# Kernel tuning notes

Measured on AMD Instinct MI355X. Metric: run time of the kernel, lower is better.

## Reference

```python
import jax, jax.numpy as jnp
import numpy as np
import math

D_MODEL = 1024
NUM_HEADS = 16
D_HEAD = D_MODEL // NUM_HEADS


def setup_inputs() -> dict:
    key = jax.random.key(0)
    k1, k2, k3, k4, k5 = jax.random.split(key, 5)
    scale = 1.0 / math.sqrt(D_MODEL)
    x = jax.random.normal(k1, (4, 2048, D_MODEL), dtype=jnp.float32)
    W_qkv = jax.random.normal(k2, (D_MODEL, 3 * D_MODEL), dtype=jnp.float32) * scale
    b_qkv = jax.random.normal(k3, (3 * D_MODEL,), dtype=jnp.float32) * 0.02
    W_o = jax.random.normal(k4, (D_MODEL, D_MODEL), dtype=jnp.float32) * scale
    b_o = jax.random.normal(k5, (D_MODEL,), dtype=jnp.float32) * 0.02
    return {"x": x, "W_qkv": W_qkv, "b_qkv": b_qkv, "W_o": W_o, "b_o": b_o}


def reference(x, W_qkv, b_qkv, W_o, b_o):
    B, C, D = x.shape
    H, Dh = NUM_HEADS, D_HEAD
    qkv = x @ W_qkv + b_qkv                       # [B, C, 3D]
    qkv = qkv.reshape(B, C, 3, H, Dh).transpose(2, 0, 3, 1, 4)  # [3, B, H, C, Dh]
    Q, K, V = qkv[0], qkv[1], qkv[2]
    scores = jnp.einsum('bhqd,bhkd->bhqk', Q, K) / math.sqrt(Dh)  # [B, H, C, C]
    causal = jnp.tril(jnp.ones((C, C), dtype=bool))
    scores = jnp.where(causal, scores, -jnp.inf)
    weights = jax.nn.softmax(scores, axis=-1)
    attn = jnp.einsum('bhqk,bhkd->bhqd', weights, V)              # [B, H, C, Dh]
    attn = attn.transpose(0, 2, 1, 3).reshape(B, C, D)
    return attn @ W_o + b_o
```

## Files before the change

kernel.cpp:

```cpp
#include <hip/hip_runtime.h>
#include <hip/hip_bf16.h>
#include <stdint.h>


typedef __attribute__((ext_vector_type(8))) short short8;
typedef __attribute__((ext_vector_type(4))) short short4v;
typedef __attribute__((ext_vector_type(4))) float f32x4;

#define AS1 __attribute__((address_space(1)))
#define AS3 __attribute__((address_space(3)))

static __device__ __forceinline__ short f2bf(float f) {
  union { float f; uint32_t u; } v; v.f = f;
  uint32_t r = v.u + 0x7fffu + ((v.u >> 16) & 1u);
  return (short)(r >> 16);
}

static __device__ __forceinline__ short f2bfh(float f) {
  __hip_bfloat16 h = __float2bfloat16(f);
  return *reinterpret_cast<short*>(&h);
}

static __device__ __forceinline__ void gload_lds16(const void* g, void* l) {
  __builtin_amdgcn_global_load_lds((const AS1 void*)g, (AS3 void*)l, 16, 0, 0);
}

__global__ __launch_bounds__(256) void k_cvt_x(const float* __restrict__ x,
                                               short* __restrict__ xb) {
  long i = ((long)blockIdx.x * 256 + threadIdx.x) * 4;
  const float4 v = *(const float4*)(x + i);
  short4v o;
  o[0] = f2bf(v.x); o[1] = f2bf(v.y); o[2] = f2bf(v.z); o[3] = f2bf(v.w);
  *(short4v*)(xb + i) = o;
}

__global__ __launch_bounds__(256) void k_transpose_bf(const float* __restrict__ W,
                                                      short* __restrict__ Wt,
                                                      int K, int N) {
  __shared__ float t[64][65];
  const int nb = blockIdx.x * 64, kb = blockIdx.y * 64;
  const int tid = threadIdx.x;
#pragma unroll
  for (int i = 0; i < 16; ++i) {
    int idx = i * 256 + tid; int r = idx >> 6, c = idx & 63;
    t[r][c] = W[(long)(kb + r) * N + nb + c];
  }
  __syncthreads();
#pragma unroll
  for (int i = 0; i < 16; ++i) {
    int idx = i * 256 + tid; int r = idx >> 6, c = idx & 63;
    Wt[(long)(nb + r) * K + kb + c] = f2bf(t[c][r]);
  }
}

template <int EPI>
__global__ __launch_bounds__(256)
void k_gemm(const short* __restrict__ A, const short* __restrict__ Bt,
            const float* __restrict__ bias, float* __restrict__ Cf,
            short* __restrict__ q_ws, short* __restrict__ k_ws, short* __restrict__ vt_ws,
            int M, int N, int K) {
  __shared__ __align__(16) short a_sh[2][128 * 32];
  __shared__ __align__(16) short b_sh[2][128 * 32];
  const int tid = threadIdx.x;
  const int lane = tid & 63, wid = tid >> 6;
  const int l15 = lane & 15, lg = lane >> 4;
  const int wr = wid >> 1, wc = wid & 1;
  const int m0 = blockIdx.y * 128, n0 = blockIdx.x * 128;

  f32x4 acc[4][4] = {};

  const int r0 = tid >> 2, g0 = tid & 3;
  const short* ga0 = A + (long)(m0 + r0) * K + g0 * 8;
  const short* gb0 = Bt + (long)(n0 + r0) * K + g0 * 8;

#define GSTAGE(buf, ks)                                                             \
  {                                                                                 \
    _Pragma("unroll")                                                               \
    for (int i = 0; i < 2; ++i) {                                                   \
      gload_lds16(ga0 + (long)i * 64 * K + (ks), &a_sh[buf][(i * 256 + tid) * 8]);  \
      gload_lds16(gb0 + (long)i * 64 * K + (ks), &b_sh[buf][(i * 256 + tid) * 8]);  \
    }                                                                               \
  }

  GSTAGE(0, 0);
  __syncthreads();

  const int nt = K >> 5;
  int cur = 0;
  for (int t = 0; t < nt; ++t) {
    if (t + 1 < nt) GSTAGE(cur ^ 1, (t + 1) * 32);

    short8 af[4], bfr[4];
#pragma unroll
    for (int m = 0; m < 4; ++m)
      af[m] = *(const short8*)(&a_sh[cur][(wr * 64 + m * 16 + l15) * 32 + lg * 8]);
#pragma unroll
    for (int n = 0; n < 4; ++n)
      bfr[n] = *(const short8*)(&b_sh[cur][(wc * 64 + n * 16 + l15) * 32 + lg * 8]);
#pragma unroll
    for (int m = 0; m < 4; ++m)
#pragma unroll
      for (int n = 0; n < 4; ++n)
        acc[m][n] = __builtin_amdgcn_mfma_f32_16x16x32_bf16(af[m], bfr[n], acc[m][n], 0, 0, 0);

    __syncthreads();
    cur ^= 1;
  }
#undef GSTAGE

#pragma unroll
  for (int mm = 0; mm < 4; ++mm) {
#pragma unroll
    for (int nn = 0; nn < 4; ++nn) {
      const int n = n0 + wc * 64 + nn * 16 + l15;
      const int mb = m0 + wr * 64 + mm * 16 + lg * 4;
      if (EPI == 1) {
#pragma unroll
        for (int r = 0; r < 4; ++r)
          Cf[(long)(mb + r) * N + n] = acc[mm][nn][r] + bias[n];
      } else {
        const int which = n >> 10;
        const int h = (n >> 6) & 15, d = n & 63;
        const int b = mb >> 11, c = mb & 2047;
        const int bh = b * 16 + h;
        const float bi = bias[n];
        if (which == 2) {
          short4v o;
#pragma unroll
          for (int r = 0; r < 4; ++r) o[r] = f2bf(acc[mm][nn][r] + bi);
          *(short4v*)(vt_ws + ((long)bh * 64 + d) * 2048 + c) = o;
        } else if (which == 0) {
#pragma unroll
          for (int r = 0; r < 4; ++r)
            q_ws[((long)bh * 2048 + c + r) * 64 + d] = f2bf((acc[mm][nn][r] + bi) * 0.125f);
        } else {
#pragma unroll
          for (int r = 0; r < 4; ++r)
            k_ws[((long)bh * 2048 + c + r) * 64 + d] = f2bf(acc[mm][nn][r] + bi);
        }
      }
    }
  }
}

__global__ __launch_bounds__(256)
void k_attn(const short* __restrict__ q_ws, const short* __restrict__ k_ws,
            const short* __restrict__ vt_ws, short* __restrict__ attn_out) {
  __shared__ __align__(16) short k_sh[2][64 * 64];
  __shared__ __align__(16) short v_sh[2][64 * 64];

  const int tid = threadIdx.x;
  const int lane = tid & 63, wid = tid >> 6;
  const int l15 = lane & 15, lg = lane >> 4;
  const int bh = blockIdx.x;
  const int qt = (int)gridDim.y - 1 - (int)blockIdx.y;
  const int b = bh >> 4, h = bh & 15;
  const int qw = qt * 64 + wid * 16;
  const int q_glob = qw + l15;

  const short* qrow = q_ws + ((long)bh * 2048 + q_glob) * 64;
  const short8 qf0 = *(const short8*)(qrow + lg * 8);
  const short8 qf1 = *(const short8*)(qrow + 32 + lg * 8);

  const int s7 = l15 & 7;
  const int koff0 = ((lg ^ s7) << 4);
  const int koff1 = (((4 + lg) ^ s7) << 4);
  const int vsub = (lg & 1) * 8, vg = lg >> 1;
  int voff[4];
#pragma unroll
  for (int m2 = 0; m2 < 4; ++m2)
    voff[m2] = (((2 * m2 + vg) ^ s7) << 4) | vsub;

  f32x4 accO[4] = {};
  float mrow = -1e30f, lrow = 0.f;

  const int srow = tid >> 3, sg = tid & 7;
  const int nkv = qt + 1;

#define STAGE(buf, kv)                                                              \
  {                                                                                 \
    _Pragma("unroll")                                                               \
    for (int i = 0; i < 2; ++i) {                                                   \
      int row = i * 32 + srow;                                                      \
      int gl = sg ^ (row & 7);                                                      \
      gload_lds16(k_ws + ((long)bh * 2048 + (kv) + row) * 64 + gl * 8,              \
                  &k_sh[buf][(i * 256 + tid) * 8]);                                 \
      gload_lds16(vt_ws + ((long)bh * 64 + row) * 2048 + (kv) + gl * 8,             \
                  &v_sh[buf][(i * 256 + tid) * 8]);                                 \
    }                                                                               \
  }

  STAGE(0, 0);
  asm volatile("s_waitcnt vmcnt(0)" ::: "memory");
  __syncthreads();

  int cur = 0;
  for (int t = 0; t < nkv; ++t) {
    const int kv0 = t * 64;
    if (t + 1 < nkv) STAGE(cur ^ 1, kv0 + 64);

    const char* ksh = (const char*)k_sh[cur];
    const char* vsh = (const char*)v_sh[cur];

    f32x4 st[4];
#pragma unroll
    for (int j = 0; j < 4; ++j) {
      const char* kr = ksh + (j * 16 + l15) * 128;
      short8 kf0 = *(const short8*)(kr + koff0);
      short8 kf1 = *(const short8*)(kr + koff1);
      f32x4 z = {};
      z = __builtin_amdgcn_mfma_f32_16x16x32_bf16(kf0, qf0, z, 0, 0, 0);
      z = __builtin_amdgcn_mfma_f32_16x16x32_bf16(kf1, qf1, z, 0, 0, 0);
      st[j] = z;
    }

    if (kv0 + 64 > qw) {
#pragma unroll
      for (int j = 0; j < 4; ++j) {
        int kvr = kv0 + j * 16 + lg * 4;
#pragma unroll
        for (int r = 0; r < 4; ++r)
          if (kvr + r > q_glob) st[j][r] = -1e30f;
      }
    }

    float a0 = fmaxf(fmaxf(st[0][0], st[0][1]), fmaxf(st[0][2], st[0][3]));
    float a1 = fmaxf(fmaxf(st[1][0], st[1][1]), fmaxf(st[1][2], st[1][3]));
    float a2 = fmaxf(fmaxf(st[2][0], st[2][1]), fmaxf(st[2][2], st[2][3]));
    float a3 = fmaxf(fmaxf(st[3][0], st[3][1]), fmaxf(st[3][2], st[3][3]));
    float mx = fmaxf(fmaxf(a0, a1), fmaxf(a2, a3));
    mx = fmaxf(mx, __shfl_xor(mx, 16));
    mx = fmaxf(mx, __shfl_xor(mx, 32));
    const float mnew = fmaxf(mrow, mx);
    const float sc = __expf(mrow - mnew);
    mrow = mnew;
    lrow *= sc;
#pragma unroll
    for (int dt = 0; dt < 4; ++dt) {
      accO[dt][0] *= sc; accO[dt][1] *= sc; accO[dt][2] *= sc; accO[dt][3] *= sc;
    }
    float ps = 0.f;
#pragma unroll
    for (int j = 0; j < 4; ++j)
#pragma unroll
      for (int r = 0; r < 4; ++r) {
        float e = __expf(st[j][r] - mnew);
        st[j][r] = e;
        ps += e;
      }
    lrow += ps;

    short8 pb0, pb1;
#pragma unroll
    for (int r = 0; r < 4; ++r) {
      pb0[r]     = f2bfh(st[0][r]);
      pb0[4 + r] = f2bfh(st[1][r]);
      pb1[r]     = f2bfh(st[2][r]);
      pb1[4 + r] = f2bfh(st[3][r]);
    }

#pragma unroll
    for (int dt = 0; dt < 4; ++dt) {
      const char* vr = vsh + (dt * 16 + l15) * 128;
      union { short8 s8; short4v s4[2]; } vf1, vf2;
      vf1.s4[0] = *(const short4v*)(vr + voff[0]);
      vf1.s4[1] = *(const short4v*)(vr + voff[1]);
      accO[dt] = __builtin_amdgcn_mfma_f32_16x16x32_bf16(vf1.s8, pb0, accO[dt], 0, 0, 0);
      vf2.s4[0] = *(const short4v*)(vr + voff[2]);
      vf2.s4[1] = *(const short4v*)(vr + voff[3]);
      accO[dt] = __builtin_amdgcn_mfma_f32_16x16x32_bf16(vf2.s8, pb1, accO[dt], 0, 0, 0);
    }

    asm volatile("s_waitcnt vmcnt(0)" ::: "memory");
    __syncthreads();
    cur ^= 1;
  }
#undef STAGE

  float lt = lrow;
  lt += __shfl_xor(lt, 16);
  lt += __shfl_xor(lt, 32);
  const float inv = 1.0f / lt;
  short* obase = attn_out + ((long)b * 2048 + q_glob) * 1024 + h * 64;
#pragma unroll
  for (int dt = 0; dt < 4; ++dt) {
    short4v o;
#pragma unroll
    for (int r = 0; r < 4; ++r) o[r] = f2bfh(accO[dt][r] * inv);
    *(short4v*)(obase + dt * 16 + lg * 4) = o;
  }
}

extern "C" void kernel_launch(void* const* d_in, const int* in_sizes, int n_in,
                              void* d_out, int out_size, void* d_ws, size_t ws_size,
                              hipStream_t stream) {
  const float* x     = (const float*)d_in[0];
  const float* W_qkv = (const float*)d_in[1];
  const float* b_qkv = (const float*)d_in[2];
  const float* W_o   = (const float*)d_in[3];
  const float* b_o   = (const float*)d_in[4];
  float* out = (float*)d_out;

  char* ws = (char*)d_ws;
  short* x_bf   = (short*)(ws);
  short* wqkv_t = (short*)(ws + 16777216);
  short* wo_t   = (short*)(ws + 23068672);
  short* q_ws   = (short*)(ws + 25165824);
  short* k_ws   = (short*)(ws + 41943040);
  short* vt_ws  = (short*)(ws + 58720256);

  k_cvt_x<<<dim3(8192), dim3(256), 0, stream>>>(x, x_bf);
  k_transpose_bf<<<dim3(48, 16), dim3(256), 0, stream>>>(W_qkv, wqkv_t, 1024, 3072);
  k_transpose_bf<<<dim3(16, 16), dim3(256), 0, stream>>>(W_o, wo_t, 1024, 1024);
  k_gemm<0><<<dim3(24, 64), dim3(256), 0, stream>>>(x_bf, wqkv_t, b_qkv, nullptr,
                                                    q_ws, k_ws, vt_ws, 8192, 3072, 1024);
  k_attn<<<dim3(64, 32), dim3(256), 0, stream>>>(q_ws, k_ws, vt_ws, x_bf);
  k_gemm<1><<<dim3(8, 64), dim3(256), 0, stream>>>(x_bf, wo_t, b_o, out,
                                                   nullptr, nullptr, nullptr, 8192, 1024, 1024);
}
```

Before: 188.3 us.

## Process two query tiles per attention block with exp2 softmax and lazy rescale

Each attention block now handles two 64-row query tiles, so every staged K/V tile in shared memory feeds both, halving K/V traffic per query. Blocks are flattened into a 1D grid with an interleaved ordering of query pairs to balance causal work across the launch. Softmax switches to exp2 by folding log2(e) into the Q scale, skips accumulator rescaling unless the running max grows by more than a threshold, and raises wave priority around the MFMA sections. This costs more registers, which may lower occupancy, and the deferred rescale relies on fp32 headroom for accuracy.

```diff
diff --git a/kernel.cpp b/kernel.cpp
--- a/kernel.cpp
+++ b/kernel.cpp
@@ -24,6 +24,8 @@
 static __device__ __forceinline__ void gload_lds16(const void* g, void* l) {
   __builtin_amdgcn_global_load_lds((const AS1 void*)g, (AS3 void*)l, 16, 0, 0);
 }
+
+#define MFMA16(a, b, c) __builtin_amdgcn_mfma_f32_16x16x32_bf16((a), (b), (c), 0, 0, 0)
 
 __global__ __launch_bounds__(256) void k_cvt_x(const float* __restrict__ x,
                                                short* __restrict__ xb) {
@@ -101,7 +103,7 @@
     for (int m = 0; m < 4; ++m)
 #pragma unroll
       for (int n = 0; n < 4; ++n)
-        acc[m][n] = __builtin_amdgcn_mfma_f32_16x16x32_bf16(af[m], bfr[n], acc[m][n], 0, 0, 0);
+        acc[m][n] = MFMA16(af[m], bfr[n], acc[m][n]);
 
     __syncthreads();
     cur ^= 1;
@@ -132,7 +134,7 @@
         } else if (which == 0) {
 #pragma unroll
           for (int r = 0; r < 4; ++r)
-            q_ws[((long)bh * 2048 + c + r) * 64 + d] = f2bf((acc[mm][nn][r] + bi) * 0.125f);
+            q_ws[((long)bh * 2048 + c + r) * 64 + d] = f2bf((acc[mm][nn][r] + bi) * 0.18033688011f);
         } else {
 #pragma unroll
           for (int r = 0; r < 4; ++r)
@@ -152,15 +154,23 @@
   const int tid = threadIdx.x;
   const int lane = tid & 63, wid = tid >> 6;
   const int l15 = lane & 15, lg = lane >> 4;
-  const int bh = blockIdx.x;
-  const int qt = (int)gridDim.y - 1 - (int)blockIdx.y;
+
+  const int n_blk = blockIdx.x;
+  const int bh = n_blk & 63;
+  const int ig = n_blk >> 6, grp = ig >> 2, k4 = ig & 3;
+  const int qp = (grp == 0) ? 15 - 4 * k4 : (grp == 1) ? 4 * k4
+               : (grp == 2) ? 14 - 4 * k4 : 1 + 4 * k4;
   const int b = bh >> 4, h = bh & 15;
-  const int qw = qt * 64 + wid * 16;
-  const int q_glob = qw + l15;
-
-  const short* qrow = q_ws + ((long)bh * 2048 + q_glob) * 64;
-  const short8 qf0 = *(const short8*)(qrow + lg * 8);
-  const short8 qf1 = *(const short8*)(qrow + 32 + lg * 8);
+  const int qw0 = qp * 128 + wid * 16;
+  const int qA = qw0 + l15, qB = qw0 + 64 + l15;
+  const int nt = 2 * qp + 2;
+
+  const short* qrowA = q_ws + ((long)bh * 2048 + qA) * 64;
+  const short* qrowB = q_ws + ((long)bh * 2048 + qB) * 64;
+  const short8 qfA0 = *(const short8*)(qrowA + lg * 8);
+  const short8 qfA1 = *(const short8*)(qrowA + 32 + lg * 8);
+  const short8 qfB0 = *(const short8*)(qrowB + lg * 8);
+  const short8 qfB1 = *(const short8*)(qrowB + 32 + lg * 8);
 
   const int s7 = l15 & 7;
   const int koff0 = ((lg ^ s7) << 4);
@@ -171,11 +181,10 @@
   for (int m2 = 0; m2 < 4; ++m2)
     voff[m2] = (((2 * m2 + vg) ^ s7) << 4) | vsub;
 
-  f32x4 accO[4] = {};
-  float mrow = -1e30f, lrow = 0.f;
+  f32x4 accA[4] = {}, accB[4] = {};
+  float mA = -1e30f, lA = 0.f, mB = -1e30f, lB = 0.f;
 
   const int srow = tid >> 3, sg = tid & 7;
-  const int nkv = qt + 1;
 
 #define STAGE(buf, kv)                                                              \
   {                                                                                 \
@@ -195,81 +204,144 @@
   __syncthreads();
 
   int cur = 0;
-  for (int t = 0; t < nkv; ++t) {
+  for (int t = 0; t < nt; ++t) {
     const int kv0 = t * 64;
-    if (t + 1 < nkv) STAGE(cur ^ 1, kv0 + 64);
+    const bool doA = (t < nt - 1);
+    if (t + 1 < nt) STAGE(cur ^ 1, kv0 + 64);
 
     const char* ksh = (const char*)k_sh[cur];
     const char* vsh = (const char*)v_sh[cur];
 
-    f32x4 st[4];
+    f32x4 stA[4], stB[4];
+    __builtin_amdgcn_s_setprio(1);
 #pragma unroll
     for (int j = 0; j < 4; ++j) {
       const char* kr = ksh + (j * 16 + l15) * 128;
       short8 kf0 = *(const short8*)(kr + koff0);
       short8 kf1 = *(const short8*)(kr + koff1);
+      if (doA) {
+        f32x4 z = {};
+        z = MFMA16(kf0, qfA0, z);
+        z = MFMA16(kf1, qfA1, z);
+        stA[j] = z;
+      }
       f32x4 z = {};
-      z = __builtin_amdgcn_mfma_f32_16x16x32_bf16(kf0, qf0, z, 0, 0, 0);
-      z = __builtin_amdgcn_mfma_f32_16x16x32_bf16(kf1, qf1, z, 0, 0, 0);
-      st[j] = z;
-    }
-
-    if (kv0 + 64 > qw) {
+      z = MFMA16(kf0, qfB0, z);
+      z = MFMA16(kf1, qfB1, z);
+      stB[j] = z;
+    }
+    __builtin_amdgcn_s_setprio(0);
+
+    if (doA && t == nt - 2) {
 #pragma unroll
       for (int j = 0; j < 4; ++j) {
         int kvr = kv0 + j * 16 + lg * 4;
 #pragma unroll
         for (int r = 0; r < 4; ++r)
-          if (kvr + r > q_glob) st[j][r] = -1e30f;
-      }
-    }
-
-    float a0 = fmaxf(fmaxf(st[0][0], st[0][1]), fmaxf(st[0][2], st[0][3]));
-    float a1 = fmaxf(fmaxf(st[1][0], st[1][1]), fmaxf(st[1][2], st[1][3]));
-    float a2 = fmaxf(fmaxf(st[2][0], st[2][1]), fmaxf(st[2][2], st[2][3]));
-    float a3 = fmaxf(fmaxf(st[3][0], st[3][1]), fmaxf(st[3][2], st[3][3]));
-    float mx = fmaxf(fmaxf(a0, a1), fmaxf(a2, a3));
-    mx = fmaxf(mx, __shfl_xor(mx, 16));
-    mx = fmaxf(mx, __shfl_xor(mx, 32));
-    const float mnew = fmaxf(mrow, mx);
-    const float sc = __expf(mrow - mnew);
-    mrow = mnew;
-    lrow *= sc;
-#pragma unroll
-    for (int dt = 0; dt < 4; ++dt) {
-      accO[dt][0] *= sc; accO[dt][1] *= sc; accO[dt][2] *= sc; accO[dt][3] *= sc;
-    }
-    float ps = 0.f;
-#pragma unroll
-    for (int j = 0; j < 4; ++j)
+          if (kvr + r > qA) stA[j][r] = -1e30f;
+      }
+    }
+    if (t == nt - 1) {
+#pragma unroll
+      for (int j = 0; j < 4; ++j) {
+        int kvr = kv0 + j * 16 + lg * 4;
+#pragma unroll
+        for (int r = 0; r < 4; ++r)
+          if (kvr + r > qB) stB[j][r] = -1e30f;
+      }
+    }
+
+    short8 pA0, pA1, pB0, pB1;
+    if (doA) {
+      float m0 = fmaxf(fmaxf(stA[0][0], stA[0][1]), fmaxf(stA[0][2], stA[0][3]));
+      float m1 = fmaxf(fmaxf(stA[1][0], stA[1][1]), fmaxf(stA[1][2], stA[1][3]));
+      float m2 = fmaxf(fmaxf(stA[2][0], stA[2][1]), fmaxf(stA[2][2], stA[2][3]));
+      float m3 = fmaxf(fmaxf(stA[3][0], stA[3][1]), fmaxf(stA[3][2], stA[3][3]));
+      float mx = fmaxf(fmaxf(m0, m1), fmaxf(m2, m3));
+      mx = fmaxf(mx, __shfl_xor(mx, 16));
+      mx = fmaxf(mx, __shfl_xor(mx, 32));
+      if (!__all(mx - mA <= 11.0f)) {
+        const float mnew = fmaxf(mA, mx);
+        const float sc = __builtin_amdgcn_exp2f(mA - mnew);
+        mA = mnew;
+        lA *= sc;
+#pragma unroll
+        for (int dt = 0; dt < 4; ++dt) {
+          accA[dt][0] *= sc; accA[dt][1] *= sc; accA[dt][2] *= sc; accA[dt][3] *= sc;
+        }
+      }
+      float ps = 0.f;
+#pragma unroll
+      for (int j = 0; j < 4; ++j)
+#pragma unroll
+        for (int r = 0; r < 4; ++r) {
+          float e = __builtin_amdgcn_exp2f(stA[j][r] - mA);
+          stA[j][r] = e;
+          ps += e;
+        }
+      lA += ps;
 #pragma unroll
       for (int r = 0; r < 4; ++r) {
-        float e = __expf(st[j][r] - mnew);
-        st[j][r] = e;
-        ps += e;
-      }
-    lrow += ps;
-
-    short8 pb0, pb1;
-#pragma unroll
-    for (int r = 0; r < 4; ++r) {
-      pb0[r]     = f2bfh(st[0][r]);
-      pb0[4 + r] = f2bfh(st[1][r]);
-      pb1[r]     = f2bfh(st[2][r]);
-      pb1[4 + r] = f2bfh(st[3][r]);
-    }
-
+        pA0[r]     = f2bfh(stA[0][r]);
+        pA0[4 + r] = f2bfh(stA[1][r]);
+        pA1[r]     = f2bfh(stA[2][r]);
+        pA1[4 + r] = f2bfh(stA[3][r]);
+      }
+    }
+    {
+      float m0 = fmaxf(fmaxf(stB[0][0], stB[0][1]), fmaxf(stB[0][2], stB[0][3]));
+      float m1 = fmaxf(fmaxf(stB[1][0], stB[1][1]), fmaxf(stB[1][2], stB[1][3]));
+      float m2 = fmaxf(fmaxf(stB[2][0], stB[2][1]), fmaxf(stB[2][2], stB[2][3]));
+      float m3 = fmaxf(fmaxf(stB[3][0], stB[3][1]), fmaxf(stB[3][2], stB[3][3]));
+      float mx = fmaxf(fmaxf(m0, m1), fmaxf(m2, m3));
+      mx = fmaxf(mx, __shfl_xor(mx, 16));
+      mx = fmaxf(mx, __shfl_xor(mx, 32));
+      if (!__all(mx - mB <= 11.0f)) {
+        const float mnew = fmaxf(mB, mx);
+        const float sc = __builtin_amdgcn_exp2f(mB - mnew);
+        mB = mnew;
+        lB *= sc;
+#pragma unroll
+        for (int dt = 0; dt < 4; ++dt) {
+          accB[dt][0] *= sc; accB[dt][1] *= sc; accB[dt][2] *= sc; accB[dt][3] *= sc;
+        }
+      }
+      float ps = 0.f;
+#pragma unroll
+      for (int j = 0; j < 4; ++j)
+#pragma unroll
+        for (int r = 0; r < 4; ++r) {
+          float e = __builtin_amdgcn_exp2f(stB[j][r] - mB);
+          stB[j][r] = e;
+          ps += e;
+        }
+      lB += ps;
+#pragma unroll
+      for (int r = 0; r < 4; ++r) {
+        pB0[r]     = f2bfh(stB[0][r]);
+        pB0[4 + r] = f2bfh(stB[1][r]);
+        pB1[r]     = f2bfh(stB[2][r]);
+        pB1[4 + r] = f2bfh(stB[3][r]);
+      }
+    }
+
+    __builtin_amdgcn_s_setprio(1);
 #pragma unroll
     for (int dt = 0; dt < 4; ++dt) {
       const char* vr = vsh + (dt * 16 + l15) * 128;
       union { short8 s8; short4v s4[2]; } vf1, vf2;
       vf1.s4[0] = *(const short4v*)(vr + voff[0]);
       vf1.s4[1] = *(const short4v*)(vr + voff[1]);
-      accO[dt] = __builtin_amdgcn_mfma_f32_16x16x32_bf16(vf1.s8, pb0, accO[dt], 0, 0, 0);
       vf2.s4[0] = *(const short4v*)(vr + voff[2]);
       vf2.s4[1] = *(const short4v*)(vr + voff[3]);
-      accO[dt] = __builtin_amdgcn_mfma_f32_16x16x32_bf16(vf2.s8, pb1, accO[dt], 0, 0, 0);
-    }
+      if (doA) {
+        accA[dt] = MFMA16(vf1.s8, pA0, accA[dt]);
+        accA[dt] = MFMA16(vf2.s8, pA1, accA[dt]);
+      }
+      accB[dt] = MFMA16(vf1.s8, pB0, accB[dt]);
+      accB[dt] = MFMA16(vf2.s8, pB1, accB[dt]);
+    }
+    __builtin_amdgcn_s_setprio(0);
 
     asm volatile("s_waitcnt vmcnt(0)" ::: "memory");
     __syncthreads();
@@ -277,17 +349,33 @@
   }
 #undef STAGE
 
-  float lt = lrow;
-  lt += __shfl_xor(lt, 16);
-  lt += __shfl_xor(lt, 32);
-  const float inv = 1.0f / lt;
-  short* obase = attn_out + ((long)b * 2048 + q_glob) * 1024 + h * 64;
-#pragma unroll
-  for (int dt = 0; dt < 4; ++dt) {
-    short4v o;
-#pragma unroll
-    for (int r = 0; r < 4; ++r) o[r] = f2bfh(accO[dt][r] * inv);
-    *(short4v*)(obase + dt * 16 + lg * 4) = o;
+  {
+    float lt = lA;
+    lt += __shfl_xor(lt, 16);
+    lt += __shfl_xor(lt, 32);
+    const float inv = 1.0f / lt;
+    short* obase = attn_out + ((long)b * 2048 + qA) * 1024 + h * 64;
+#pragma unroll
+    for (int dt = 0; dt < 4; ++dt) {
+      short4v o;
+#pragma unroll
+      for (int r = 0; r < 4; ++r) o[r] = f2bfh(accA[dt][r] * inv);
+      *(short4v*)(obase + dt * 16 + lg * 4) = o;
+    }
+  }
+  {
+    float lt = lB;
+    lt += __shfl_xor(lt, 16);
+    lt += __shfl_xor(lt, 32);
+    const float inv = 1.0f / lt;
+    short* obase = attn_out + ((long)b * 2048 + qB) * 1024 + h * 64;
+#pragma unroll
+    for (int dt = 0; dt < 4; ++dt) {
+      short4v o;
+#pragma unroll
+      for (int r = 0; r < 4; ++r) o[r] = f2bfh(accB[dt][r] * inv);
+      *(short4v*)(obase + dt * 16 + lg * 4) = o;
+    }
   }
 }
 
@@ -314,7 +402,7 @@
   k_transpose_bf<<<dim3(16, 16), dim3(256), 0, stream>>>(W_o, wo_t, 1024, 1024);
   k_gemm<0><<<dim3(24, 64), dim3(256), 0, stream>>>(x_bf, wqkv_t, b_qkv, nullptr,
                                                     q_ws, k_ws, vt_ws, 8192, 3072, 1024);
-  k_attn<<<dim3(64, 32), dim3(256), 0, stream>>>(q_ws, k_ws, vt_ws, x_bf);
+  k_attn<<<dim3(1024), dim3(256), 0, stream>>>(q_ws, k_ws, vt_ws, x_bf);
   k_gemm<1><<<dim3(8, 64), dim3(256), 0, stream>>>(x_bf, wo_t, b_o, out,
                                                    nullptr, nullptr, nullptr, 8192, 1024, 1024);
 }
```

Result: slower. 209.1 us (+11.1%).
